# Performance work log

Measured on AMD Instinct MI355X. Metric: run time of the kernel, lower is better.

The kernel has to match this reference:

```python
import jax, jax.numpy as jnp
import numpy as np
import math
from jax import lax

IN_C = 512
OUT_C = 512
K = 3
GROUPS = 1
EXP_NITER = 5
MAXC = max(IN_C, OUT_C)
PAD_A = int(math.ceil((K - 1) / 2))  # left/top pad
PAD_B = int(math.floor((K - 1) / 2))  # right/bottom pad


def pad_fct(x):
    # ConstantPad2d((ceil, floor, ceil, floor), 0) on last two dims
    return jnp.pad(x, ((0, 0), (0, 0), (PAD_A, PAD_B), (PAD_A, PAD_B)))


def fast_matrix_conv(m1, m2, groups=1):
    # m1: (m, n, k1, k2); m2: (nb, m//groups, l1, l2)
    # composes two conv kernels: result (nb, n, k+l-1, k+l-1)
    m, n, k1, k2 = m1.shape
    nb, mb, l1, l2 = m2.shape
    x = jnp.transpose(m1, (1, 0, 2, 3))          # (n, m, k1, k2) -> batch=n, chan=m
    w = jnp.flip(m2, (-2, -1))                   # true convolution via flip
    r = lax.conv_general_dilated(
        x, w, window_strides=(1, 1),
        padding=[(l1 - 1, l1 - 1), (l2 - 1, l2 - 1)],
        dimension_numbers=("NCHW", "OIHW", "NCHW"),
        feature_group_count=groups,
    )                                            # (n, nb, k1+l1-1, k2+l2-1)
    return jnp.transpose(r, (1, 0, 2, 3))


def identity_kernel():
    gic = MAXC // GROUPS
    eye = jnp.eye(gic, dtype=jnp.float32)[:, :, None, None]     # (gic, gic, 1, 1)
    eye = jnp.tile(eye[None], (GROUPS, 1, 1, 1, 1)).reshape(MAXC, gic, 1, 1)
    return pad_fct(eye)                                          # (MAXC, gic, K, K)


def setup_inputs() -> dict:
    key = jax.random.key(0)
    kernel = jax.random.normal(key, (MAXC, MAXC // GROUPS, K, K), dtype=jnp.float32) * 0.05
    return {"kernel": kernel}


def reference(kernel):
    kg = kernel + identity_kernel()
    ki = kernel
    for i in range(2, EXP_NITER + 1):
        ki = fast_matrix_conv(ki, kernel, GROUPS) / float(i)
        kg = pad_fct(kg) + ki
    g = GROUPS
    kh, kw = kg.shape[-2], kg.shape[-1]
    kg = kg.reshape(g, MAXC // g, MAXC // g, kh, kw)
    kg = kg[:, : OUT_C // g, : IN_C // g, :, :]
    return kg.reshape(OUT_C, IN_C // g, kh, kw)
```

## Files before the change

### kernel.cpp

```cpp
#include <hip/hip_runtime.h>
#include <stdint.h>

#define C 512
#define C2 262144

typedef __attribute__((ext_vector_type(8))) short bf16x8;
typedef __attribute__((ext_vector_type(4))) float f32x4;

__device__ __forceinline__ unsigned short f2bf(float f) {
    union { float f; uint32_t u; } v; v.f = f;
    uint32_t u = v.u;
    u += 0x7fffu + ((u >> 16) & 1u);
    return (unsigned short)(u >> 16);
}
__device__ __forceinline__ float bf2f(unsigned short h) {
    union { uint32_t u; float f; } v; v.u = ((uint32_t)h) << 16;
    return v.f;
}

#define GL2LDS16(g, l) __builtin_amdgcn_global_load_lds( \
    (const __attribute__((address_space(1))) void*)(g),  \
    (__attribute__((address_space(3))) void*)(l), 16, 0, 0)

__device__ __forceinline__ bf16x8 ldsr16(const char* p) {
    bf16x8 r;
    asm volatile("ds_read_b128 %0, %1"
                 : "=v"(r)
                 : "v"((__attribute__((address_space(3))) const void*)p));
    return r;
}

__device__ __forceinline__ int nth_valid(int mask, int n) {
    int pq = 0;
    while (true) {
        if (mask & 1) { if (n == 0) return pq; --n; }
        mask >>= 1; ++pq;
    }
}

__global__ void k_transform(const float* __restrict__ K,
                            unsigned short* __restrict__ Kt,
                            unsigned short* __restrict__ KtT,
                            float* __restrict__ Ktf) {
    int t = blockIdx.x * 256 + threadIdx.x;
    int a = t >> 9, b = t & 511;
#pragma unroll
    for (int j = 0; j < 9; ++j) {
        float v = K[(size_t)t * 9 + j];
        unsigned short h = f2bf(v);
        Kt[(size_t)j * C2 + t] = h;
        KtT[(size_t)j * C2 + (size_t)b * C + a] = h;
        Ktf[(size_t)j * C2 + (size_t)b * C + a] = v;
    }
}

__global__ void k_sched(int* __restrict__ sched) {
    __shared__ int hist[4][10];
    __shared__ int base[4][10];
    const int tid = threadIdx.x;
    if (tid < 40) ((int*)hist)[tid] = 0;
    if (tid < 4) sched[tid] = 0;
    __syncthreads();
    const int offs[5] = {0, 25, 74, 155, 276};
    int step = -1, yx = 0, V = 0;
    if (tid < 276) {
#pragma unroll
        for (int s = 0; s < 4; ++s)
            if (tid >= offs[s] && tid < offs[s + 1]) { step = s; yx = tid - offs[s]; }
        const int s_out = 5 + 2 * step, s_in = s_out - 2;
        const int y = yx / s_out, x = yx % s_out;
        int vy = 0, vx = 0;
#pragma unroll
        for (int p = 0; p < 3; ++p) {
            if (y - p >= 0 && y - p < s_in) ++vy;
            if (x - p >= 0 && x - p < s_in) ++vx;
        }
        V = vy * vx;
        atomicAdd(&hist[step][V], 1);
    }
    __syncthreads();
    if (tid < 4) {
        int acc = 0;
        for (int v = 9; v >= 1; --v) { base[tid][v] = acc; acc += hist[tid][v]; }
        for (int v = 1; v <= 9; ++v) hist[tid][v] = 0;
    }
    __syncthreads();
    if (tid < 276) {
        const int idx = atomicAdd(&hist[step][V], 1);
        sched[4 + step * 484 + base[step][V] + idx] = yx;
    }
}

__global__ __launch_bounds__(256, 2) void k_gemm(
    const unsigned short* __restrict__ A,
    const unsigned short* __restrict__ Bm,
    unsigned short* __restrict__ Out,
    int s_in, int s_out, float alpha,
    int* __restrict__ ctr, const int* __restrict__ list, int n_items)
{
    __shared__ __align__(16) char lds[65536];
    __shared__ int s_item;

    const int tid = threadIdx.x;
    const int lane = tid & 63, wid = tid >> 6;
    const int wr = wid >> 1, wc = wid & 1;
    const int l15 = lane & 15, lhi = lane >> 4;

    const int soff = (tid >> 3) * 1024 + ((((tid & 7) ^ ((tid >> 3) & 7))) << 4);
    const int t16 = tid * 16;

    const int coff0 = ((lhi ^ (l15 & 7)) << 4);
    const int coff1 = (((lhi + 4) ^ (l15 & 7)) << 4);
    const int arow = (wr * 64 + l15) * 128;
    const int brow = (wc * 64 + l15) * 128;

    const char* Abase = (const char*)A;
    const char* Bbase = (const char*)Bm;

#define STAGE4(SRC, SLOT) { \
        const char* s_ = (SRC) + soff; \
        GL2LDS16(s_,         lds + (SLOT) + t16); \
        GL2LDS16(s_ + 32768, lds + (SLOT) + 4096 + t16); \
        GL2LDS16(s_ + 65536, lds + (SLOT) + 8192 + t16); \
        GL2LDS16(s_ + 98304, lds + (SLOT) + 12288 + t16); \
    }

    for (;;) {
        __syncthreads();
        if (tid == 0) s_item = atomicAdd(ctr, 1);
        __syncthreads();
        const int itm = s_item;
        if (itm >= n_items) break;
        const int yx = list[itm >> 4];
        const int quad = itm & 15;
        const int i0 = (quad & 3) * 128, o0 = (quad >> 2) * 128;
        const int y = yx / s_out, x = yx % s_out;

        int mask = 0, V = 0;
        for (int pq = 0; pq < 9; ++pq) {
            int u = y - pq / 3, v = x - pq % 3;
            if (u >= 0 && u < s_in && v >= 0 && v < s_in) { mask |= 1 << pq; ++V; }
        }

        auto slabA = [&](int pq) {
            int u = y - pq / 3, v = x - pq % 3;
            return Abase + ((size_t)(u * s_in + v) * C + i0) * (size_t)(C * 2);
        };
        auto slabB = [&](int pq) {
            return Bbase + ((size_t)pq * C + o0) * (size_t)(C * 2);
        };
        const int pq0 = nth_valid(mask, 0);
        const char* curA = slabA(pq0);
        const char* curB = slabB(pq0);
        const char* nxtA = curA;
        const char* nxtB = curB;
        if (V > 1) { int p1 = nth_valid(mask, 1); nxtA = slabA(p1); nxtB = slabB(p1); }

        f32x4 acc[4][4] = {};
        bf16x8 bBa[8], bBb[8];
        bf16x8 aE[4], aO[4];

        STAGE4(curB,       0)
        STAGE4(curA,       16384)
        STAGE4(curB + 128, 32768)
        STAGE4(curA + 128, 49152)
        asm volatile("s_waitcnt vmcnt(8)" ::: "memory");
        __builtin_amdgcn_s_barrier();
        __builtin_amdgcn_sched_barrier(0);
#pragma unroll
        for (int n = 0; n < 4; ++n) {
            bBa[n * 2 + 0] = ldsr16(lds + brow + n * 2048 + coff0);
            bBa[n * 2 + 1] = ldsr16(lds + brow + n * 2048 + coff1);
        }
#pragma unroll
        for (int mi = 0; mi < 2; ++mi) {
            aE[mi * 2 + 0] = ldsr16(lds + 16384 + arow + mi * 2048 + coff0);
            aE[mi * 2 + 1] = ldsr16(lds + 16384 + arow + mi * 2048 + coff1);
        }
        asm volatile("s_waitcnt lgkmcnt(0)" ::: "memory");
        __builtin_amdgcn_s_barrier();
        __builtin_amdgcn_sched_barrier(0);

        const int NI = 4 * V;
        for (int it = 0; it < NI; ++it) {
            const int itl = it & 3;
            const bool lastq = (itl == 3);
            const bool dummy = lastq && (((it >> 2) + 1) >= V);
            const char* sAe = lastq ? nxtA : curA;
            const char* sBe = lastq ? nxtB : curB;
            const int cse = lastq ? 0 : (2 * itl + 2) * 128;
            const int cso = cse + 128;

#define PHASE(PH) { \
        constexpr int apar_  = ((PH) == 1 || (PH) == 2) ? 1 : 0; \
        constexpr int apair_ = ((PH) == 0 || (PH) == 2) ? 1 : 0; \
        constexpr int aslot_ = apar_ ? 49152 : 16384; \
         \
        _Pragma("unroll") for (int mi = 0; mi < 2; ++mi) { \
            bf16x8 t0 = ldsr16(lds + aslot_ + arow + apair_ * 4096 + mi * 2048 + coff0); \
            bf16x8 t1 = ldsr16(lds + aslot_ + arow + apair_ * 4096 + mi * 2048 + coff1); \
            if constexpr (((PH) & 1) == 0) { aO[mi * 2 + 0] = t0; aO[mi * 2 + 1] = t1; } \
            else                           { aE[mi * 2 + 0] = t0; aE[mi * 2 + 1] = t1; } \
        } \
         \
        if constexpr ((PH) == 1 || (PH) == 3) { \
            constexpr int bslot_ = ((PH) == 1) ? 32768 : 0; \
            _Pragma("unroll") for (int n = 0; n < 4; ++n) { \
                bf16x8 t0 = ldsr16(lds + bslot_ + brow + n * 2048 + coff0); \
                bf16x8 t1 = ldsr16(lds + bslot_ + brow + n * 2048 + coff1); \
                if constexpr ((PH) == 1) { bBb[n * 2 + 0] = t0; bBb[n * 2 + 1] = t1; } \
                else                     { bBa[n * 2 + 0] = t0; bBa[n * 2 + 1] = t1; } \
            } \
        } \
        asm volatile("" ::: "memory"); \
        if (!dummy) { \
            if constexpr ((PH) == 0) STAGE4(sBe + cse, 0)       \
            if constexpr ((PH) == 1) STAGE4(sAe + cse, 16384)   \
            if constexpr ((PH) == 2) STAGE4(sBe + cso, 32768)   \
            if constexpr ((PH) == 3) STAGE4(sAe + cso, 49152)   \
        } \
        __builtin_amdgcn_sched_barrier(0); \
        __builtin_amdgcn_s_setprio(1); \
        _Pragma("unroll") for (int mi = 0; mi < 2; ++mi) \
        _Pragma("unroll") for (int n = 0; n < 4; ++n) { \
            if constexpr (((PH) & 1) == 0 && (PH) < 2) { \
                acc[mi][n] = __builtin_amdgcn_mfma_f32_16x16x32_bf16(aE[mi*2+0], bBa[n*2+0], acc[mi][n], 0, 0, 0); \
                acc[mi][n] = __builtin_amdgcn_mfma_f32_16x16x32_bf16(aE[mi*2+1], bBa[n*2+1], acc[mi][n], 0, 0, 0); \
            } else if constexpr (((PH) & 1) == 1 && (PH) < 2) { \
                acc[2+mi][n] = __builtin_amdgcn_mfma_f32_16x16x32_bf16(aO[mi*2+0], bBa[n*2+0], acc[2+mi][n], 0, 0, 0); \
                acc[2+mi][n] = __builtin_amdgcn_mfma_f32_16x16x32_bf16(aO[mi*2+1], bBa[n*2+1], acc[2+mi][n], 0, 0, 0); \
            } else if constexpr (((PH) & 1) == 0) { \
                acc[mi][n] = __builtin_amdgcn_mfma_f32_16x16x32_bf16(aE[mi*2+0], bBb[n*2+0], acc[mi][n], 0, 0, 0); \
                acc[mi][n] = __builtin_amdgcn_mfma_f32_16x16x32_bf16(aE[mi*2+1], bBb[n*2+1], acc[mi][n], 0, 0, 0); \
            } else { \
                acc[2+mi][n] = __builtin_amdgcn_mfma_f32_16x16x32_bf16(aO[mi*2+0], bBb[n*2+0], acc[2+mi][n], 0, 0, 0); \
                acc[2+mi][n] = __builtin_amdgcn_mfma_f32_16x16x32_bf16(aO[mi*2+1], bBb[n*2+1], acc[2+mi][n], 0, 0, 0); \
            } \
        } \
        __builtin_amdgcn_s_setprio(0); \
        asm volatile("s_waitcnt lgkmcnt(0)" ::: "memory"); \
        if constexpr ((PH) == 0 || (PH) == 2) { \
            if (dummy) { asm volatile("s_waitcnt vmcnt(0)" ::: "memory"); } \
            else       { asm volatile("s_waitcnt vmcnt(4)" ::: "memory"); } \
        } \
        __builtin_amdgcn_s_barrier(); \
        __builtin_amdgcn_sched_barrier(0); \
    }

            PHASE(0) PHASE(1) PHASE(2) PHASE(3)
#undef PHASE

            if (lastq) {
                curA = nxtA; curB = nxtB;
                int vn = (it >> 2) + 2;
                if (vn < V) {
                    int pqn = nth_valid(mask, vn);
                    nxtA = slabA(pqn); nxtB = slabB(pqn);
                }
            }
        }

#pragma unroll
        for (int M = 0; M < 4; ++M) {
#pragma unroll
            for (int r = 0; r < 4; ++r) {
                const int irow = i0 + wr * 64 + M * 16 + lhi * 4 + r;
                unsigned short* op = Out + ((size_t)yx * C + irow) * C
                                   + o0 + wc * 64 + l15;
#pragma unroll
                for (int n = 0; n < 4; ++n)
                    op[n * 16] = f2bf(acc[M][n][r] * alpha);
            }
        }
    }
#undef STAGE4
    asm volatile("s_waitcnt vmcnt(0)" ::: "memory");
}

__global__ __launch_bounds__(256) void k_final(
    const unsigned short* __restrict__ Ka, int sa, int ofa,
    const unsigned short* __restrict__ Kb, int sb, int ofb,
    const float* __restrict__ Ktf, float* __restrict__ kg, int init)
{
    __shared__ float L[64 * 121];
    const int i = blockIdx.x;
    const int o0 = blockIdx.y * 64;
    const int tid = threadIdx.x, lane = tid & 63, wid = tid >> 6;

    for (int idx = tid; idx < 64 * 121; idx += 256) L[idx] = 0.f;
    __syncthreads();

    const int sa2 = sa * sa;
    for (int yxv = wid; yxv < sa2; yxv += 4) {
        float v = bf2f(Ka[((size_t)yxv * C + i) * C + o0 + lane]);
        int yy = yxv / sa + ofa, xx = yxv % sa + ofa;
        L[lane * 121 + yy * 11 + xx] += v;
    }
    __syncthreads();
    const int sb2 = sb * sb;
    for (int yxv = wid; yxv < sb2; yxv += 4) {
        float v = bf2f(Kb[((size_t)yxv * C + i) * C + o0 + lane]);
        int yy = yxv / sb + ofb, xx = yxv % sb + ofb;
        L[lane * 121 + yy * 11 + xx] += v;
    }
    __syncthreads();
    if (init) {
        for (int j = wid; j < 9; j += 4) {
            float v = Ktf[(size_t)j * C2 + (size_t)i * C + o0 + lane];
            if (j == 4 && (o0 + lane) == i) v += 1.0f;
            L[lane * 121 + (j / 3 + 4) * 11 + (j % 3 + 4)] += v;
        }
    }
    __syncthreads();
    if (init) {
        for (int idx = tid; idx < 64 * 121; idx += 256) {
            int ol = idx / 121, w = idx - ol * 121;
            kg[((size_t)(o0 + ol) * C + i) * 121 + w] = L[idx];
        }
    } else {
        for (int idx = tid; idx < 64 * 121; idx += 256) {
            int ol = idx / 121, w = idx - ol * 121;
            kg[((size_t)(o0 + ol) * C + i) * 121 + w] += L[idx];
        }
    }
}

__global__ __launch_bounds__(256) void k_final4(
    const unsigned short* __restrict__ K2, const unsigned short* __restrict__ K3,
    const unsigned short* __restrict__ K4, const unsigned short* __restrict__ K5,
    const float* __restrict__ Ktf, float* __restrict__ kg)
{
    __shared__ float L[64 * 121];
    const int i = blockIdx.x;
    const int o0 = blockIdx.y * 64;
    const int tid = threadIdx.x, lane = tid & 63, wid = tid >> 6;

    for (int idx = tid; idx < 64 * 121; idx += 256) L[idx] = 0.f;
    __syncthreads();

#define ADDSRC(SRC, S, OFS) { \
        const int s2_ = (S) * (S); \
        for (int yxv = wid; yxv < s2_; yxv += 4) { \
            float v = bf2f((SRC)[((size_t)yxv * C + i) * C + o0 + lane]); \
            int yy = yxv / (S) + (OFS), xx = yxv % (S) + (OFS); \
            L[lane * 121 + yy * 11 + xx] += v; \
        } \
        __syncthreads(); \
    }
    ADDSRC(K2, 5, 3) ADDSRC(K3, 7, 2) ADDSRC(K4, 9, 1) ADDSRC(K5, 11, 0)
#undef ADDSRC

    for (int j = wid; j < 9; j += 4) {
        float v = Ktf[(size_t)j * C2 + (size_t)i * C + o0 + lane];
        if (j == 4 && (o0 + lane) == i) v += 1.0f;
        L[lane * 121 + (j / 3 + 4) * 11 + (j % 3 + 4)] += v;
    }
    __syncthreads();
    for (int idx = tid; idx < 64 * 121; idx += 256) {
        int ol = idx / 121, w = idx - ol * 121;
        kg[((size_t)(o0 + ol) * C + i) * 121 + w] = L[idx];
    }
}

extern "C" void kernel_launch(void* const* d_in, const int* in_sizes, int n_in,
                              void* d_out, int out_size, void* d_ws, size_t ws_size,
                              hipStream_t stream) {
    const float* K = (const float*)d_in[0];
    float* kg = (float*)d_out;
    char* ws = (char*)d_ws;

    unsigned short* Kt  = (unsigned short*)(ws);
    unsigned short* KtT = (unsigned short*)(ws + (size_t)4718592);
    float*          Ktf = (float*)         (ws + (size_t)9437184);

    const bool big = (ws_size >= (size_t)163585616);

    if (big) {
        unsigned short* Ki2 = (unsigned short*)(ws + (size_t)18874368);
        unsigned short* Ki3 = (unsigned short*)(ws + (size_t)31981568);
        unsigned short* Ki4 = (unsigned short*)(ws + (size_t)57671680);
        unsigned short* Ki5 = (unsigned short*)(ws + (size_t)100139008);
        int* sch = (int*)(ws + (size_t)163577856);
        int* ctr = sch;
        int* lst = sch + 4;

        k_transform<<<1024, 256, 0, stream>>>(K, Kt, KtT, Ktf);
        k_sched<<<1, 320, 0, stream>>>(sch);
        k_gemm<<<512, 256, 0, stream>>>(KtT, Kt, Ki2, 3, 5, 0.5f,
                                        ctr + 0, lst + 0 * 484, 400);
        k_gemm<<<512, 256, 0, stream>>>(Ki2, Kt, Ki3, 5, 7, 1.0f / 3.0f,
                                        ctr + 1, lst + 1 * 484, 784);
        k_gemm<<<512, 256, 0, stream>>>(Ki3, Kt, Ki4, 7, 9, 0.25f,
                                        ctr + 2, lst + 2 * 484, 1296);
        k_gemm<<<512, 256, 0, stream>>>(Ki4, Kt, Ki5, 9, 11, 0.2f,
                                        ctr + 3, lst + 3 * 484, 1936);
        k_final4<<<dim3(512, 8), 256, 0, stream>>>(Ki2, Ki3, Ki4, Ki5, Ktf, kg);
    } else {
        unsigned short* P1 = (unsigned short*)(ws + (size_t)18874368);
        unsigned short* P2 = (unsigned short*)(ws + (size_t)61341696);
        int* sch = (int*)(ws + (size_t)124780544);
        int* ctr = sch;
        int* lst = sch + 4;

        k_transform<<<1024, 256, 0, stream>>>(K, Kt, KtT, Ktf);
        k_sched<<<1, 320, 0, stream>>>(sch);
        k_gemm<<<512, 256, 0, stream>>>(KtT, Kt, P1, 3, 5, 0.5f,
                                        ctr + 0, lst + 0 * 484, 400);
        k_gemm<<<512, 256, 0, stream>>>(P1, Kt, P2, 5, 7, 1.0f / 3.0f,
                                        ctr + 1, lst + 1 * 484, 784);
        k_final<<<dim3(512, 8), 256, 0, stream>>>(P1, 5, 3, P2, 7, 2, Ktf, kg, 1);
        k_gemm<<<512, 256, 0, stream>>>(P2, Kt, P1, 7, 9, 0.25f,
                                        ctr + 2, lst + 2 * 484, 1296);
        k_gemm<<<512, 256, 0, stream>>>(P1, Kt, P2, 9, 11, 0.2f,
                                        ctr + 3, lst + 3 * 484, 1936);
        k_final<<<dim3(512, 8), 256, 0, stream>>>(P1, 9, 1, P2, 11, 0, Ktf, kg, 0);
    }
}
```

Before: 538.4 us.

## Load B operand directly from global into registers, halving LDS staging

The GEMM kernel no longer stages the B (weight) tiles through LDS. Each lane now issues global_load_dwordx4 straight into its MFMA operand registers, interleaved across the four phases, with reworked vmcnt waits. LDS shrinks from 64KB to 32KB and holds only the A tiles. The aim is to cut LDS traffic and footprint, which could allow higher occupancy. The cost is uncoalesced per-lane global reads of B, redundant B loads across waves, and global latency exposed directly in the MFMA pipeline.

Result: slower. 1.000 ms (+85.8%).

```diff
diff --git a/kernel.cpp b/kernel.cpp
--- a/kernel.cpp
+++ b/kernel.cpp
@@ -27,6 +27,14 @@
     asm volatile("ds_read_b128 %0, %1"
                  : "=v"(r)
                  : "v"((__attribute__((address_space(3))) const void*)p));
+    return r;
+}
+
+__device__ __forceinline__ bf16x8 gld16(const char* p) {
+    bf16x8 r;
+    asm volatile("global_load_dwordx4 %0, %1, off"
+                 : "=&v"(r)
+                 : "v"((const __attribute__((address_space(1))) void*)p));
     return r;
 }
 
@@ -98,7 +106,7 @@
     int s_in, int s_out, float alpha,
     int* __restrict__ ctr, const int* __restrict__ list, int n_items)
 {
-    __shared__ __align__(16) char lds[65536];
+    __shared__ __align__(16) char lds[32768];
     __shared__ int s_item;
 
     const int tid = threadIdx.x;
@@ -112,7 +120,7 @@
     const int coff0 = ((lhi ^ (l15 & 7)) << 4);
     const int coff1 = (((lhi + 4) ^ (l15 & 7)) << 4);
     const int arow = (wr * 64 + l15) * 128;
-    const int brow = (wc * 64 + l15) * 128;
+    const int bglane = (wc * 64 + l15) * 1024 + lhi * 16;
 
     const char* Abase = (const char*)A;
     const char* Bbase = (const char*)Bm;
@@ -160,22 +168,20 @@
         bf16x8 bBa[8], bBb[8];
         bf16x8 aE[4], aO[4];
 
-        STAGE4(curB,       0)
-        STAGE4(curA,       16384)
-        STAGE4(curB + 128, 32768)
-        STAGE4(curA + 128, 49152)
-        asm volatile("s_waitcnt vmcnt(8)" ::: "memory");
+        STAGE4(curA,       0)
+        STAGE4(curA + 128, 16384)
+#pragma unroll
+        for (int n = 0; n < 4; ++n)
+#pragma unroll
+            for (int h = 0; h < 2; ++h)
+                bBa[n * 2 + h] = gld16(curB + bglane + n * 16384 + h * 64);
+        asm volatile("s_waitcnt vmcnt(0)" ::: "memory");
         __builtin_amdgcn_s_barrier();
         __builtin_amdgcn_sched_barrier(0);
 #pragma unroll
-        for (int n = 0; n < 4; ++n) {
-            bBa[n * 2 + 0] = ldsr16(lds + brow + n * 2048 + coff0);
-            bBa[n * 2 + 1] = ldsr16(lds + brow + n * 2048 + coff1);
-        }
-#pragma unroll
         for (int mi = 0; mi < 2; ++mi) {
-            aE[mi * 2 + 0] = ldsr16(lds + 16384 + arow + mi * 2048 + coff0);
-            aE[mi * 2 + 1] = ldsr16(lds + 16384 + arow + mi * 2048 + coff1);
+            aE[mi * 2 + 0] = ldsr16(lds + arow + mi * 2048 + coff0);
+            aE[mi * 2 + 1] = ldsr16(lds + arow + mi * 2048 + coff1);
         }
         asm volatile("s_waitcnt lgkmcnt(0)" ::: "memory");
         __builtin_amdgcn_s_barrier();
@@ -188,13 +194,14 @@
             const bool dummy = lastq && (((it >> 2) + 1) >= V);
             const char* sAe = lastq ? nxtA : curA;
             const char* sBe = lastq ? nxtB : curB;
-            const int cse = lastq ? 0 : (2 * itl + 2) * 128;
-            const int cso = cse + 128;
+            const int c1b  = (2 * itl + 1) * 128;
+            const int cseb = lastq ? 0 : (2 * itl + 2) * 128;
+            const int csob = cseb + 128;
 
 #define PHASE(PH) { \
         constexpr int apar_  = ((PH) == 1 || (PH) == 2) ? 1 : 0; \
         constexpr int apair_ = ((PH) == 0 || (PH) == 2) ? 1 : 0; \
-        constexpr int aslot_ = apar_ ? 49152 : 16384; \
+        constexpr int aslot_ = apar_ ? 16384 : 0; \
          \
         _Pragma("unroll") for (int mi = 0; mi < 2; ++mi) { \
             bf16x8 t0 = ldsr16(lds + aslot_ + arow + apair_ * 4096 + mi * 2048 + coff0); \
@@ -203,22 +210,21 @@
             else                           { aE[mi * 2 + 0] = t0; aE[mi * 2 + 1] = t1; } \
         } \
          \
-        if constexpr ((PH) == 1 || (PH) == 3) { \
-            constexpr int bslot_ = ((PH) == 1) ? 32768 : 0; \
-            _Pragma("unroll") for (int n = 0; n < 4; ++n) { \
-                bf16x8 t0 = ldsr16(lds + bslot_ + brow + n * 2048 + coff0); \
-                bf16x8 t1 = ldsr16(lds + bslot_ + brow + n * 2048 + coff1); \
-                if constexpr ((PH) == 1) { bBb[n * 2 + 0] = t0; bBb[n * 2 + 1] = t1; } \
-                else                     { bBa[n * 2 + 0] = t0; bBa[n * 2 + 1] = t1; } \
+        if constexpr ((PH) == 0) { \
+            _Pragma("unroll") for (int n = 0; n < 4; ++n) \
+            _Pragma("unroll") for (int h = 0; h < 2; ++h) \
+                bBb[n * 2 + h] = gld16(curB + c1b + bglane + n * 16384 + h * 64); \
+        } \
+        if constexpr ((PH) == 2) { \
+            if (!dummy) { \
+                _Pragma("unroll") for (int n = 0; n < 4; ++n) \
+                _Pragma("unroll") for (int h = 0; h < 2; ++h) \
+                    bBa[n * 2 + h] = gld16(sBe + cseb + bglane + n * 16384 + h * 64); \
             } \
         } \
         asm volatile("" ::: "memory"); \
-        if (!dummy) { \
-            if constexpr ((PH) == 0) STAGE4(sBe + cse, 0)       \
-            if constexpr ((PH) == 1) STAGE4(sAe + cse, 16384)   \
-            if constexpr ((PH) == 2) STAGE4(sBe + cso, 32768)   \
-            if constexpr ((PH) == 3) STAGE4(sAe + cso, 49152)   \
-        } \
+        if constexpr ((PH) == 1) { if (!dummy) STAGE4(sAe + cseb, 0) }       \
+        if constexpr ((PH) == 3) { if (!dummy) STAGE4(sAe + csob, 16384) }   \
         __builtin_amdgcn_sched_barrier(0); \
         __builtin_amdgcn_s_setprio(1); \
         _Pragma("unroll") for (int mi = 0; mi < 2; ++mi) \
@@ -239,7 +245,18 @@
         } \
         __builtin_amdgcn_s_setprio(0); \
         asm volatile("s_waitcnt lgkmcnt(0)" ::: "memory"); \
-        if constexpr ((PH) == 0 || (PH) == 2) { \
+        if constexpr ((PH) == 0) { \
+            asm volatile("s_waitcnt vmcnt(8)" ::: "memory"); \
+        } \
+        if constexpr ((PH) == 1) { \
+            if (dummy) { asm volatile("s_waitcnt vmcnt(0)" ::: "memory"); } \
+            else       { asm volatile("s_waitcnt vmcnt(4)" ::: "memory"); } \
+        } \
+        if constexpr ((PH) == 2) { \
+            if (dummy) { asm volatile("s_waitcnt vmcnt(0)" ::: "memory"); } \
+            else       { asm volatile("s_waitcnt vmcnt(8)" ::: "memory"); } \
+        } \
+        if constexpr ((PH) == 3) { \
             if (dummy) { asm volatile("s_waitcnt vmcnt(0)" ::: "memory"); } \
             else       { asm volatile("s_waitcnt vmcnt(4)" ::: "memory"); } \
         } \
```
